# Performance work log

Hardware: AMD Instinct MI355X
Metric: run time of the kernel (lower is better)

The kernel has to match this reference:

```python
import jax, jax.numpy as jnp
import numpy as np

H_OUT, W_OUT = 473, 473  # original image size the logits are upsampled to
BN_EPS = 1e-5


def _conv(x, w, pad):
    return jax.lax.conv_general_dilated(
        x, w, window_strides=(1, 1), padding=[(pad, pad), (pad, pad)],
        dimension_numbers=('NCHW', 'OIHW', 'NCHW'))


def _bn(x, g, b):
    # BatchNorm2d in training mode: batch statistics over (N, H, W)
    m = jnp.mean(x, axis=(0, 2, 3), keepdims=True)
    v = jnp.var(x, axis=(0, 2, 3), keepdims=True)
    return (x - m) * jax.lax.rsqrt(v + BN_EPS) * g.reshape(1, -1, 1, 1) + b.reshape(1, -1, 1, 1)


def setup_inputs() -> dict:
    key = jax.random.key(0)
    ks = jax.random.split(key, 8)
    B, C, Hf, Wf, NC = 2, 256, 60, 60, 2
    return {
        'V_a': jax.random.normal(ks[0], (B, C, Hf, Wf), jnp.float32),
        'V_b': jax.random.normal(ks[1], (B, C, Hf, Wf), jnp.float32),
        'D_a': jax.random.normal(ks[2], (B, C, Hf, Wf), jnp.float32),
        'W_e': jax.random.normal(ks[3], (C, C), jnp.float32) * 0.02,
        'gate_w': jax.random.normal(ks[4], (1, C, 1, 1), jnp.float32) * 0.01,
        'conv1_w': jax.random.normal(ks[5], (C, 3 * C, 3, 3), jnp.float32) * 0.01,
        'conv2_w': jax.random.normal(ks[6], (C, 2 * C, 3, 3), jnp.float32) * 0.01,
        'bn1_g': jnp.ones((C,), jnp.float32),
        'bn1_b': jnp.zeros((C,), jnp.float32),
        'bn2_g': jnp.ones((C,), jnp.float32),
        'bn2_b': jnp.zeros((C,), jnp.float32),
        'cls1_w': jax.random.normal(ks[7], (NC, C, 1, 1), jnp.float32) * 0.01,
        'cls1_b': jnp.zeros((NC,), jnp.float32),
        'cls2_w': jax.random.normal(jax.random.fold_in(key, 9), (NC, C, 1, 1), jnp.float32) * 0.01,
        'cls2_b': jnp.zeros((NC,), jnp.float32),
    }


def reference(V_a, V_b, D_a, W_e, gate_w, conv1_w, conv2_w,
              bn1_g, bn1_b, bn2_g, bn2_b, cls1_w, cls1_b, cls2_w, cls2_b):
    B, C, Hf, Wf = V_a.shape
    N = Hf * Wf
    V_a_flat = V_a.reshape(B, C, N)
    V_b_flat = V_b.reshape(B, C, N)

    # linear_e on transposed A features, then affinity S = (A^T W^T) B
    weighted = jnp.einsum('bcn,dc->bnd', V_a_flat, W_e)        # [B, N, C]
    S = jnp.einsum('bnd,bdm->bnm', weighted, V_b_flat)         # [B, N, N]

    S_row = jax.nn.softmax(S, axis=1)                          # softmax over dim 1
    S_colT = jax.nn.softmax(jnp.swapaxes(S, 1, 2), axis=1)     # softmax of S^T over dim 1

    Z_b = jnp.einsum('bcn,bnm->bcm', V_a_flat, S_row)          # attended for view b
    Z_a = jnp.einsum('bcn,bnm->bcm', V_b_flat, S_colT)         # attended for view a

    att1 = Z_a.reshape(B, C, Hf, Wf)
    att2 = Z_b.reshape(B, C, Hf, Wf)

    # 1x1 sigmoid gates
    att1 = att1 * jax.nn.sigmoid(_conv(att1, gate_w, 0))
    att2 = att2 * jax.nn.sigmoid(_conv(att2, gate_w, 0))

    # conc1: branch-1 concatenates gated attention, RGB feat, and depth feat
    x1 = jnp.concatenate([att1, V_a, D_a], axis=1)             # [B, 3C, Hf, Wf]
    x2 = jnp.concatenate([att2, V_b], axis=1)                  # [B, 2C, Hf, Wf]

    x1 = jax.nn.relu(_bn(_conv(x1, conv1_w, 1), bn1_g, bn1_b))
    x2 = jax.nn.relu(_bn(_conv(x2, conv2_w, 1), bn2_g, bn2_b))

    x1 = _conv(x1, cls1_w, 0) + cls1_b.reshape(1, -1, 1, 1)
    x2 = _conv(x2, cls2_w, 0) + cls2_b.reshape(1, -1, 1, 1)

    NC = cls1_w.shape[0]
    x1 = jax.image.resize(x1, (B, NC, H_OUT, W_OUT), 'linear')
    x2 = jax.image.resize(x2, (B, NC, H_OUT, W_OUT), 'linear')
    return jax.nn.sigmoid(x1), jax.nn.sigmoid(x2)
```

## Files before the change

kernel.cpp:

```cpp
#include <hip/hip_runtime.h>

#define BB 2
#define CC 256
#define NN 3600
#define NCH 2
#define HO 473
#define WO 473
#define NR 3712
#define NTI 29
#define ZKI 29
#define ZKS 4
#define CZKS 3

typedef unsigned short u16;
typedef __attribute__((ext_vector_type(8))) short short8;
typedef __attribute__((ext_vector_type(4))) float f32x4;

static __device__ __forceinline__ u16 f2bf(float f) {
    unsigned u = __float_as_uint(f);
    unsigned r = (u + 0x7FFF + ((u >> 16) & 1)) >> 16;
    return (u16)r;
}
static __device__ __forceinline__ u16 f2h(float f) {
    _Float16 h = (_Float16)f;
    return __builtin_bit_cast(unsigned short, h);
}
static __device__ __forceinline__ float h2f(u16 u) {
    _Float16 h = __builtin_bit_cast(_Float16, u);
    return (float)h;
}

static __device__ __forceinline__ void glds16(const u16* g, u16* l) {
    __builtin_amdgcn_global_load_lds(
        (const __attribute__((address_space(1))) void*)g,
        (__attribute__((address_space(3))) void*)l, 16, 0, 0);
}


__global__ __launch_bounds__(256)
void gemm_we(const u16* __restrict__ vat, const u16* __restrict__ web,
             u16* __restrict__ wgtb)
{
    __shared__ u16 As[128 * 64];
    __shared__ u16 Bs[128 * 64];
    const u16* A = vat + (long)blockIdx.z * NR * CC;
    u16* Cp = wgtb + (long)blockIdx.z * NR * CC;

    const int t = threadIdx.x;
    const int w = t >> 6, lane = t & 63;
    const int mh = (w >> 1) * 64, nh = (w & 1) * 64;
    const int lm = lane & 15, quad = lane >> 4;
    const int m0 = blockIdx.y * 128, n0 = blockIdx.x * 128;
    const int wb = t & 192;

    f32x4 acc[4][4] = {};

    for (int k0 = 0; k0 < CC; k0 += 64) {
#pragma unroll
        for (int i = 0; i < 4; ++i) {
            int idx = i * 256 + t;
            int row = idx >> 3;
            int sc8 = ((idx ^ row) & 7) * 8;
            glds16(A + (long)(m0 + row) * CC + k0 + sc8, &As[(i * 256 + wb) * 8]);
            glds16(web + (long)(n0 + row) * CC + k0 + sc8, &Bs[(i * 256 + wb) * 8]);
        }
        __syncthreads();
#pragma unroll
        for (int s = 0; s < 2; ++s) {
            short8 a[4], b[4];
#pragma unroll
            for (int i = 0; i < 4; ++i)
                a[i] = *(const short8*)(&As[(mh + i * 16 + lm) * 64 + ((s * 4 + quad) ^ (lm & 7)) * 8]);
#pragma unroll
            for (int j = 0; j < 4; ++j)
                b[j] = *(const short8*)(&Bs[(nh + j * 16 + lm) * 64 + ((s * 4 + quad) ^ (lm & 7)) * 8]);
#pragma unroll
            for (int i = 0; i < 4; ++i)
#pragma unroll
                for (int j = 0; j < 4; ++j)
                    acc[i][j] = __builtin_amdgcn_mfma_f32_16x16x32_bf16(a[i], b[j], acc[i][j], 0, 0, 0);
        }
        __syncthreads();
    }
#pragma unroll
    for (int i = 0; i < 4; ++i)
#pragma unroll
        for (int r = 0; r < 4; ++r) {
            int row = m0 + mh + i * 16 + quad * 4 + r;
            if (row < NN)
#pragma unroll
                for (int j = 0; j < 4; ++j) {
                    int col = n0 + nh + j * 16 + lm;
                    if (col < CC) Cp[(long)row * CC + col] = f2bf(acc[i][j][r]);
                }
        }
}

__global__ __launch_bounds__(256)
void gemm_s_stats(const u16* __restrict__ A, const u16* __restrict__ B,
                  u16* __restrict__ Sh, u16* __restrict__ STh,
                  float* __restrict__ prowm, float* __restrict__ prows,
                  float* __restrict__ pcolm, float* __restrict__ pcols)
{
    __shared__ u16 smem[17408];
    u16* As = smem;
    u16* Bs = smem + 8192;

    const int t = threadIdx.x;
    const int w = t >> 6, lane = t & 63;
    const int mh = (w >> 1) * 64, nh = (w & 1) * 64;
    const int lm = lane & 15, quad = lane >> 4;
    const int m0 = blockIdx.y * 128, n0 = blockIdx.x * 128;
    const int wb = t & 192;

    f32x4 acc[4][4] = {};

    for (int k0 = 0; k0 < CC; k0 += 64) {
#pragma unroll
        for (int i = 0; i < 4; ++i) {
            int idx = i * 256 + t;
            int row = idx >> 3;
            int sc8 = ((idx ^ row) & 7) * 8;
            glds16(A + (long)(m0 + row) * CC + k0 + sc8, &As[(i * 256 + wb) * 8]);
            glds16(B + (long)(n0 + row) * CC + k0 + sc8, &Bs[(i * 256 + wb) * 8]);
        }
        __syncthreads();
#pragma unroll
        for (int s = 0; s < 2; ++s) {
            short8 a[4], b[4];
#pragma unroll
            for (int i = 0; i < 4; ++i)
                a[i] = *(const short8*)(&As[(mh + i * 16 + lm) * 64 + ((s * 4 + quad) ^ (lm & 7)) * 8]);
#pragma unroll
            for (int j = 0; j < 4; ++j)
                b[j] = *(const short8*)(&Bs[(nh + j * 16 + lm) * 64 + ((s * 4 + quad) ^ (lm & 7)) * 8]);
#pragma unroll
            for (int i = 0; i < 4; ++i)
#pragma unroll
                for (int j = 0; j < 4; ++j)
                    acc[i][j] = __builtin_amdgcn_mfma_f32_16x16x32_bf16(a[i], b[j], acc[i][j], 0, 0, 0);
        }
        __syncthreads();
    }

    u16* tr = smem;

#pragma unroll
    for (int i = 0; i < 4; ++i)
#pragma unroll
        for (int j = 0; j < 4; ++j)
#pragma unroll
            for (int r = 0; r < 4; ++r)
                tr[(mh + i * 16 + quad * 4 + r) * 136 + (nh + j * 16 + lm)] = f2h(acc[i][j][r]);
    __syncthreads();
    {
        int row = t >> 1, hf = t & 1;
        int ng = m0 + row;
        if (ng < NN) {
#pragma unroll
            for (int q = 0; q < 8; ++q) {
                int cb = n0 + hf * 64 + q * 8;
                if (cb < NN)
                    *(uint4*)(&Sh[(long)ng * NR + cb]) =
                        *(const uint4*)(&tr[row * 136 + hf * 64 + q * 8]);
            }
        }
    }
    __syncthreads();

    bool cval[4];
#pragma unroll
    for (int j = 0; j < 4; ++j) cval[j] = (n0 + nh + j * 16 + lm) < NN;

    float* sm = (float*)smem;
    float* rowm = sm;
    float* rows_ = sm + 256;
    float* colm = sm + 512;
    float* cols_ = sm + 768;

#pragma unroll
    for (int i = 0; i < 4; ++i)
#pragma unroll
        for (int r = 0; r < 4; ++r) {
            float m = -3.0e38f;
#pragma unroll
            for (int j = 0; j < 4; ++j) if (cval[j]) m = fmaxf(m, acc[i][j][r]);
            m = fmaxf(m, __shfl_xor(m, 1, 64));
            m = fmaxf(m, __shfl_xor(m, 2, 64));
            m = fmaxf(m, __shfl_xor(m, 4, 64));
            m = fmaxf(m, __shfl_xor(m, 8, 64));
            float s = 0.f;
#pragma unroll
            for (int j = 0; j < 4; ++j) if (cval[j]) s += __expf(acc[i][j][r] - m);
            s += __shfl_xor(s, 1, 64);
            s += __shfl_xor(s, 2, 64);
            s += __shfl_xor(s, 4, 64);
            s += __shfl_xor(s, 8, 64);
            if (lm == 0) {
                int rr = mh + i * 16 + quad * 4 + r;
                rowm[(w & 1) * 128 + rr] = m;
                rows_[(w & 1) * 128 + rr] = s;
            }
        }

#pragma unroll
    for (int j = 0; j < 4; ++j) {
        float m = -3.0e38f;
#pragma unroll
        for (int i = 0; i < 4; ++i)
#pragma unroll
            for (int r = 0; r < 4; ++r)
                if (m0 + mh + i * 16 + quad * 4 + r < NN) m = fmaxf(m, acc[i][j][r]);
        m = fmaxf(m, __shfl_xor(m, 16, 64));
        m = fmaxf(m, __shfl_xor(m, 32, 64));
        float s = 0.f;
#pragma unroll
        for (int i = 0; i < 4; ++i)
#pragma unroll
            for (int r = 0; r < 4; ++r)
                if (m0 + mh + i * 16 + quad * 4 + r < NN) s += __expf(acc[i][j][r] - m);
        s += __shfl_xor(s, 16, 64);
        s += __shfl_xor(s, 32, 64);
        if (quad == 0) {
            int ccl = nh + j * 16 + lm;
            colm[(w >> 1) * 128 + ccl] = m;
            cols_[(w >> 1) * 128 + ccl] = s;
        }
    }
    __syncthreads();

    if (t < 128) {
        float m1 = rowm[t], m2 = rowm[128 + t];
        float M = fmaxf(m1, m2);
        float s = rows_[t] * __expf(m1 - M) + rows_[128 + t] * __expf(m2 - M);
        if (m0 + t < NN) {
            prowm[(long)blockIdx.x * NR + m0 + t] = M;
            prows[(long)blockIdx.x * NR + m0 + t] = s;
        }
    } else {
        int c = t - 128;
        float m1 = colm[c], m2 = colm[128 + c];
        float M = fmaxf(m1, m2);
        float s = cols_[c] * __expf(m1 - M) + cols_[128 + c] * __expf(m2 - M);
        if (n0 + c < NN) {
            pcolm[(long)blockIdx.y * NR + n0 + c] = M;
            pcols[(long)blockIdx.y * NR + n0 + c] = s;
        }
    }

    __syncthreads();
#pragma unroll
    for (int i = 0; i < 4; ++i)
#pragma unroll
        for (int j = 0; j < 4; ++j)
#pragma unroll
            for (int r = 0; r < 4; ++r)
                tr[(nh + j * 16 + lm) * 136 + (mh + i * 16 + quad * 4 + r)] = f2h(acc[i][j][r]);
    __syncthreads();
    {
        int row = t >> 1, hf = t & 1;
        int mg = n0 + row;
        if (mg < NN) {
#pragma unroll
            for (int q = 0; q < 8; ++q) {
                int cb = m0 + hf * 64 + q * 8;
                if (cb < NN)
                    *(uint4*)(&STh[(long)mg * NR + cb]) =
                        *(const uint4*)(&tr[row * 136 + hf * 64 + q * 8]);
            }
        }
    }
}

__global__ __launch_bounds__(256)
void stats_final(const float* __restrict__ prm, const float* __restrict__ prs,
                 const float* __restrict__ pcm, const float* __restrict__ pcs,
                 float* __restrict__ rm, float* __restrict__ ri,
                 float* __restrict__ cm, float* __restrict__ ci)
{
    int i = blockIdx.x * 256 + threadIdx.x;
    if (i >= NN) return;
    const float* pm = blockIdx.y ? pcm : prm;
    const float* ps = blockIdx.y ? pcs : prs;
    float m = -3.0e38f, s = 0.f;
#pragma unroll 4
    for (int tI = 0; tI < NTI; ++tI) {
        float m2 = pm[(long)tI * NR + i], s2 = ps[(long)tI * NR + i];
        float M = fmaxf(m, m2);
        s = s * __expf(m - M) + s2 * __expf(m2 - M);
        m = M;
    }
    float inv = 1.f / s;
    if (blockIdx.y) { cm[i] = m; ci[i] = inv; }
    else            { rm[i] = m; ri[i] = inv; }
}

__global__ __launch_bounds__(256, 2)
void gemm_z_128(const u16* __restrict__ vab_b, const u16* __restrict__ vbb_b,
                const u16* __restrict__ STh, const u16* __restrict__ Sh,
                const float* __restrict__ rm, const float* __restrict__ ri,
                const float* __restrict__ cm, const float* __restrict__ ci,
                float* __restrict__ Zb_b, float* __restrict__ Za_b)
{
    __shared__ u16 As[128 * 128];
    __shared__ u16 Bs[128 * 128];

    const int t = threadIdx.x;
    const int w = t >> 6, lane = t & 63;
    const int mh = (w >> 1) * 64, nh = (w & 1) * 64;
    const int lm = lane & 15, quad = lane >> 4;
    const int n0 = blockIdx.x * 128;
    const int ks = blockIdx.y;
    const int zz = blockIdx.z;
    const int branch = zz & 1;
    const int m0 = (zz >> 1) * 128;
    const u16* A = branch ? vbb_b : vab_b;
    const u16* B = branch ? Sh : STh;
    const float* mxp = branch ? rm : cm;
    const float* isp = branch ? ri : ci;
    float* Cp = branch ? Za_b : Zb_b;
    const int wb = t & 192;

    const int base = ZKI / ZKS, rem = ZKI % ZKS;
    const int it0 = ks * base + (ks < rem ? ks : rem);
    const int itn = base + (ks < rem ? 1 : 0);

    int scv[8];
    const u16* Arow[8];
    const u16* Brow[8];
    float bm[8], bi[8];
#pragma unroll
    for (int i = 0; i < 8; ++i) {
        int idx = i * 256 + t;
        int row = idx >> 4, c = idx & 15;
        scv[i] = (c & 8) * 8 + ((c ^ row) & 7) * 8;
        Arow[i] = A + (long)(m0 + row) * NR + scv[i];
        int rg = n0 + row;
        Brow[i] = B + (long)rg * NR + scv[i];
        int rc = rg < NN ? rg : 0;
        bm[i] = mxp[rc];
        bi[i] = isp[rc];
    }

    f32x4 acc[4][4] = {};

    for (int it = it0; it < it0 + itn; ++it) {
        const int k0 = it * 128;
#pragma unroll
        for (int i = 0; i < 8; ++i)
            glds16(Arow[i] + k0, &As[(i * 256 + wb) * 8]);
#pragma unroll
        for (int i = 0; i < 8; ++i) {
            u16 o[8];
            uint4 v = *(const uint4*)(Brow[i] + k0);
            const u16* hp = (const u16*)&v;
            if (k0 + scv[i] < NN) {
#pragma unroll
                for (int e = 0; e < 8; ++e)
                    o[e] = f2bf(__expf(h2f(hp[e]) - bm[i]) * bi[i]);
            } else {
#pragma unroll
                for (int e = 0; e < 8; ++e) o[e] = 0;
            }
            *(uint4*)(&Bs[(i * 256 + t) * 8]) = *(const uint4*)o;
        }
        __syncthreads();
#pragma unroll
        for (int s = 0; s < 4; ++s) {
            const int sl = ((s >> 1) * 8 + (((s & 1) * 4 + quad) ^ (lm & 7))) * 8;
            short8 a[4], b[4];
#pragma unroll
            for (int i = 0; i < 4; ++i)
                a[i] = *(const short8*)(&As[(mh + i * 16 + lm) * 128 + sl]);
#pragma unroll
            for (int j = 0; j < 4; ++j)
                b[j] = *(const short8*)(&Bs[(nh + j * 16 + lm) * 128 + sl]);
#pragma unroll
            for (int i = 0; i < 4; ++i)
#pragma unroll
                for (int j = 0; j < 4; ++j)
                    acc[i][j] = __builtin_amdgcn_mfma_f32_16x16x32_bf16(a[i], b[j], acc[i][j], 0, 0, 0);
        }
        __syncthreads();
    }

#pragma unroll
    for (int i = 0; i < 4; ++i)
#pragma unroll
        for (int r = 0; r < 4; ++r) {
            int row = m0 + mh + i * 16 + quad * 4 + r;
#pragma unroll
            for (int j = 0; j < 4; ++j) {
                int col = n0 + nh + j * 16 + lm;
                if (col < NN)
                    atomicAdd(&Cp[(long)row * NN + col], acc[i][j][r]);
            }
        }
}

__global__ __launch_bounds__(256, 4)
void conv_both(const u16* __restrict__ W1, const u16* __restrict__ W2,
               const u16* __restrict__ gzaT, const u16* __restrict__ vat,
               const u16* __restrict__ daT, const u16* __restrict__ gzbT,
               const u16* __restrict__ vbt, const u16* __restrict__ zbuf,
               float* __restrict__ y1, float* __restrict__ y2)
{
    __shared__ u16 As[128 * 64];
    __shared__ u16 Bs[128 * 64];

    const int t = threadIdx.x;
    const int w = t >> 6, lane = t & 63;
    const int mh = (w >> 1) * 64, nh = (w & 1) * 64;
    const int lm = lane & 15, quad = lane >> 4;
    const int wb = t & 192;

    const long L = blockIdx.x + (long)NTI * (blockIdx.y + (long)CZKS * blockIdx.z);
    const int combo = (int)(L & 7);
    const long rest = L >> 3;
    const int ks = (int)(rest % CZKS);
    const int px = (int)(rest / CZKS);
    const int which = combo >> 2;
    const int b = (combo >> 1) & 1;
    const int m0 = (combo & 1) * 128;
    const int n0 = px * 128;

    const int CIN = which ? 512 : 768;
    const int KT = 9 * CIN;
    const u16* W = which ? W2 : W1;
    const u16* P0 = which ? gzbT : gzaT;
    const u16* P1 = which ? vbt : vat;
    const u16* P2 = which ? vbt : daT;
    float* Y = which ? y2 : y1;
    const long pstride = (long)NR * CC;

    const int PER = 3 * (CIN / 64);
    const int it0 = ks * PER;
    const int dh = ks - 1;

    int rowv[4], sc8v[4], rb[4];
    bool okd[4][3];
#pragma unroll
    for (int i = 0; i < 4; ++i) {
        int idx = i * 256 + t;
        int row = idx >> 3;
        rowv[i] = row;
        sc8v[i] = ((idx ^ row) & 7) * 8;
        int pq = n0 + row;
        int h = pq / 60, wp = pq - h * 60;
        rb[i] = (pq + dh * 60) * CC + sc8v[i];
        bool hok = (pq < NN) && ((unsigned)(h + dh) < 60u);
#pragma unroll
        for (int d = 0; d < 3; ++d)
            okd[i][d] = hok && ((unsigned)(wp + d - 1) < 60u);
    }

    f32x4 acc[4][4] = {};

    for (int it = it0; it < it0 + PER; ++it) {
        const int k0 = it * 64;
        const int g = it - it0;
        const int dw = g % 3;
        const int pc = g / 3;
        const int plane = pc >> 2;
        const int cip = (pc & 3) * 64;
        const u16* srcp = ((plane == 0) ? P0 : (plane == 1) ? P1 : P2)
                          + (long)b * pstride + cip;

#pragma unroll
        for (int i = 0; i < 4; ++i) {
            glds16(W + (long)(m0 + rowv[i]) * KT + k0 + sc8v[i], &As[(i * 256 + wb) * 8]);
            const u16* gs = okd[i][dw] ? srcp + rb[i] + (dw - 1) * CC : zbuf;
            glds16(gs, &Bs[(i * 256 + wb) * 8]);
        }
        __syncthreads();
#pragma unroll
        for (int s = 0; s < 2; ++s) {
            short8 a[4], bfr[4];
#pragma unroll
            for (int i = 0; i < 4; ++i)
                a[i] = *(const short8*)(&As[(mh + i * 16 + lm) * 64 + ((s * 4 + quad) ^ (lm & 7)) * 8]);
#pragma unroll
            for (int j = 0; j < 4; ++j)
                bfr[j] = *(const short8*)(&Bs[(nh + j * 16 + lm) * 64 + ((s * 4 + quad) ^ (lm & 7)) * 8]);
#pragma unroll
            for (int i = 0; i < 4; ++i)
#pragma unroll
                for (int j = 0; j < 4; ++j)
                    acc[i][j] = __builtin_amdgcn_mfma_f32_16x16x32_bf16(a[i], bfr[j], acc[i][j], 0, 0, 0);
        }
        __syncthreads();
    }

    float* out = Y + (long)b * CC * NN;
#pragma unroll
    for (int i = 0; i < 4; ++i)
#pragma unroll
        for (int r = 0; r < 4; ++r) {
            int row = m0 + mh + i * 16 + quad * 4 + r;
#pragma unroll
            for (int j = 0; j < 4; ++j) {
                int col = n0 + nh + j * 16 + lm;
                if (col < NN)
                    atomicAdd(&out[(long)row * NN + col], acc[i][j][r]);
            }
        }
}

__global__ __launch_bounds__(256)
void cvt_we(const float* __restrict__ W, u16* __restrict__ O)
{
    int i = blockIdx.x * 256 + threadIdx.x;
    if (i < CC * CC) O[i] = f2bf(W[i]);
}

__global__ __launch_bounds__(256)
void transpose_cvt3(const float* __restrict__ Va, const float* __restrict__ Vb,
                    const float* __restrict__ Da,
                    u16* __restrict__ vat, u16* __restrict__ vbt,
                    u16* __restrict__ daT,
                    u16* __restrict__ vab, u16* __restrict__ vbb)
{
    __shared__ float tile[64][65];
    int z = blockIdx.z;
    int s = z % 3, b = z / 3;
    const float* V = (s == 0) ? Va : (s == 1) ? Vb : Da;
    u16* VT = (s == 0) ? vat : (s == 1) ? vbt : daT;
    u16* Vpad = (s == 0) ? vab : (s == 1) ? vbb : nullptr;

    int c0 = blockIdx.y * 64, n0 = blockIdx.x * 64;
    int t = threadIdx.x;
#pragma unroll
    for (int e = 0; e < 16; ++e) {
        int f = e * 256 + t; int i = f >> 6, j = f & 63;
        int n = n0 + j;
        float v = 0.f;
        if (n < NN) v = V[((long)b * CC + c0 + i) * NN + n];
        tile[i][j] = v;
        if (Vpad) Vpad[((long)b * CC + c0 + i) * NR + n] = f2bf(v);
    }
    __syncthreads();
#pragma unroll
    for (int e = 0; e < 16; ++e) {
        int f = e * 256 + t; int i = f >> 6, j = f & 63;
        int n = n0 + i;
        if (n < NN) VT[((long)b * NR + n) * CC + c0 + j] = f2bf(tile[j][i]);
    }
}

__global__ __launch_bounds__(256)
void transpose_gate(const float* __restrict__ Za, const float* __restrict__ Zb,
                    const float* __restrict__ sga, const float* __restrict__ sgb,
                    u16* __restrict__ gzaT, u16* __restrict__ gzbT)
{
    __shared__ float tile[64][65];
    int z = blockIdx.z;
    int b = z & 1, ab = z >> 1;
    const float* Z = ab ? Zb : Za;
    const float* sg = ab ? sgb : sga;
    u16* ZT = ab ? gzbT : gzaT;

    int c0 = blockIdx.y * 64, n0 = blockIdx.x * 64;
    int t = threadIdx.x;
#pragma unroll
    for (int e = 0; e < 16; ++e) {
        int f = e * 256 + t; int i = f >> 6, j = f & 63;
        int n = n0 + j;
        float v = 0.f;
        if (n < NN) v = Z[((long)b * CC + c0 + i) * NN + n];
        tile[i][j] = v;
    }
    __syncthreads();
#pragma unroll
    for (int e = 0; e < 16; ++e) {
        int f = e * 256 + t; int i = f >> 6, j = f & 63;
        int n = n0 + i;
        if (n < NN)
            ZT[((long)b * NR + n) * CC + c0 + j] = f2bf(tile[j][i] * sg[b * NN + n]);
    }
}

template<int CIN>
__global__ __launch_bounds__(256)
void cvt_convw(const float* __restrict__ W, u16* __restrict__ O)
{
    const int KT = 9 * CIN;
    const int PER = 3 * (CIN / 64);
    long idx = (long)blockIdx.x * 256 + threadIdx.x;
    if (idx >= (long)CC * KT) return;
    int co = (int)(idx / KT);
    int r = (int)(idx % KT);
    int c64 = r >> 6, within = r & 63;
    int ks = c64 / PER, g = c64 % PER;
    int dw = g % 3, pc = g / 3;
    int tap = ks * 3 + dw;
    int ci = pc * 64 + within;
    O[idx] = f2bf(W[((long)co * CIN + ci) * 9 + tap]);
}

__global__ __launch_bounds__(256)
void gate_sig(const float* __restrict__ Za, const float* __restrict__ Zb,
              const float* __restrict__ gw,
              float* __restrict__ sga, float* __restrict__ sgb)
{
    int t = threadIdx.x;
    int px = t & 63, ck = t >> 6;
    int b = blockIdx.y;
    int ab = blockIdx.z;
    const float* Z = ab ? Zb : Za;
    float* sg = ab ? sgb : sga;
    int p = blockIdx.x * 64 + px;
    const float* Zp = Z + (long)b * CC * NN;
    float g = 0.f;
    if (p < NN) {
        for (int c = ck * 64; c < ck * 64 + 64; ++c) g += gw[c] * Zp[(long)c * NN + p];
    }
    __shared__ float red[256];
    red[t] = g;
    __syncthreads();
    if (t < 64) {
        int pp = blockIdx.x * 64 + t;
        if (pp < NN) {
            float tot = red[t] + red[t + 64] + red[t + 128] + red[t + 192];
            sg[b * NN + pp] = 1.f / (1.f + __expf(-tot));
        }
    }
}

__global__ __launch_bounds__(256)
void bn_stats_kernel(const float* __restrict__ y1, const float* __restrict__ y2,
                     const float* __restrict__ g1, const float* __restrict__ b1,
                     const float* __restrict__ g2, const float* __restrict__ b2,
                     float* __restrict__ sc1, float* __restrict__ sh1,
                     float* __restrict__ sc2, float* __restrict__ sh2)
{
    int which = blockIdx.x >> 8;
    int c = blockIdx.x & 255, t = threadIdx.x;
    const float* Y = which ? y2 : y1;
    const float* g = which ? g2 : g1;
    const float* beta = which ? b2 : b1;
    float* scale = which ? sc2 : sc1;
    float* shift = which ? sh2 : sh1;
    float s = 0.f, sq = 0.f;
    for (int b = 0; b < BB; ++b) {
        const float* p = Y + (long)b * CC * NN + (long)c * NN;
        for (int i = t; i < NN; i += 256) { float v = p[i]; s += v; sq += v * v; }
    }
    __shared__ float ls[256], lq[256];
    ls[t] = s; lq[t] = sq;
    __syncthreads();
    for (int off = 128; off > 0; off >>= 1) {
        if (t < off) { ls[t] += ls[t + off]; lq[t] += lq[t + off]; }
        __syncthreads();
    }
    if (t == 0) {
        const float inv = 1.f / (float)(BB * NN);
        float mean = ls[0] * inv;
        float var = fmaxf(lq[0] * inv - mean * mean, 0.f);
        float sc = g[c] * rsqrtf(var + 1e-5f);
        scale[c] = sc;
        shift[c] = beta[c] - mean * sc;
    }
}

__global__ __launch_bounds__(256)
void cls_kernel(const float* __restrict__ y1, const float* __restrict__ y2,
                const float* __restrict__ sc1, const float* __restrict__ sh1,
                const float* __restrict__ sc2, const float* __restrict__ sh2,
                const float* __restrict__ cw1, const float* __restrict__ cb1,
                const float* __restrict__ cw2, const float* __restrict__ cb2,
                float* __restrict__ O1, float* __restrict__ O2)
{
    int which = blockIdx.z;
    const float* Y = which ? y2 : y1;
    const float* scale = which ? sc2 : sc1;
    const float* shift = which ? sh2 : sh1;
    const float* cw = which ? cw2 : cw1;
    const float* cb = which ? cb2 : cb1;
    float* O = which ? O2 : O1;

    int t = threadIdx.x;
    int px = t & 63, ck = t >> 6;
    int b = blockIdx.y;
    int p = blockIdx.x * 64 + px;
    const float* Yb = Y + (long)b * CC * NN;
    float a0 = 0.f, a1 = 0.f;
    if (p < NN) {
        for (int c = ck * 64; c < ck * 64 + 64; ++c) {
            float v = Yb[(long)c * NN + p] * scale[c] + shift[c];
            v = fmaxf(v, 0.f);
            a0 += cw[c] * v;
            a1 += cw[CC + c] * v;
        }
    }
    __shared__ float r0[256], r1[256];
    r0[t] = a0; r1[t] = a1;
    __syncthreads();
    if (t < 64) {
        int pp = blockIdx.x * 64 + t;
        if (pp < NN) {
            float s0 = r0[t] + r0[t + 64] + r0[t + 128] + r0[t + 192];
            float s1 = r1[t] + r1[t + 64] + r1[t + 128] + r1[t + 192];
            O[(long)b * NCH * NN + pp] = s0 + cb[0];
            O[(long)b * NCH * NN + NN + pp] = s1 + cb[1];
        }
    }
}

__global__ __launch_bounds__(256)
void resize_sig_kernel(const float* __restrict__ I1, const float* __restrict__ I2,
                       float* __restrict__ O)
{
    const long HALF = (long)BB * NCH * HO * WO;
    long gid = (long)blockIdx.x * 256 + threadIdx.x;
    if (gid >= HALF) return;
    int half = blockIdx.y;
    const float* I = half ? I2 : I1;
    float* Op = O + half * HALF;

    int j = (int)(gid % WO);
    long r = gid / WO;
    int i = (int)(r % HO);
    int pc = (int)(r / HO);
    const float* ip = I + (long)pc * NN;

    const float SCL = 60.0f / 473.0f;
    float fy = (i + 0.5f) * SCL - 0.5f;
    float fx = (j + 0.5f) * SCL - 0.5f;
    int y0 = (int)floorf(fy);
    int x0 = (int)floorf(fx);
    float ty = fy - (float)y0;
    float tx = fx - (float)x0;
    int y0c = max(y0, 0), y1c = min(y0 + 1, 59);
    int x0c = max(x0, 0), x1c = min(x0 + 1, 59);
    float va = ip[y0c * 60 + x0c], vb = ip[y0c * 60 + x1c];
    float vc = ip[y1c * 60 + x0c], vd = ip[y1c * 60 + x1c];
    float v = (1.f - ty) * ((1.f - tx) * va + tx * vb) + ty * ((1.f - tx) * vc + tx * vd);
    Op[gid] = 1.f / (1.f + __expf(-v));
}

extern "C" void kernel_launch(void* const* d_in, const int* in_sizes, int n_in,
                              void* d_out, int out_size, void* d_ws, size_t ws_size,
                              hipStream_t stream)
{
    const float* V_a    = (const float*)d_in[0];
    const float* V_b    = (const float*)d_in[1];
    const float* D_a    = (const float*)d_in[2];
    const float* W_e    = (const float*)d_in[3];
    const float* gate_w = (const float*)d_in[4];
    const float* conv1_w = (const float*)d_in[5];
    const float* conv2_w = (const float*)d_in[6];
    const float* bn1_g = (const float*)d_in[7];
    const float* bn1_b = (const float*)d_in[8];
    const float* bn2_g = (const float*)d_in[9];
    const float* bn2_b = (const float*)d_in[10];
    const float* cls1_w = (const float*)d_in[11];
    const float* cls1_b = (const float*)d_in[12];
    const float* cls2_w = (const float*)d_in[13];
    const float* cls2_b = (const float*)d_in[14];
    float* out = (float*)d_out;

    size_t off = 0;
    char* wsb = (char*)d_ws;
    auto carve = [&](size_t bytes) -> char* {
        char* p = wsb + off; off += (bytes + 255) & ~(size_t)255; return p;
    };

    u16* Sh    = (u16*)carve((size_t)NR * NR * 2);
    u16* STh   = (u16*)carve((size_t)NR * NR * 2);
    u16* vab   = (u16*)carve((size_t)BB * CC * NR * 2);
    u16* vbb   = (u16*)carve((size_t)BB * CC * NR * 2);
    u16* vat   = (u16*)carve((size_t)BB * NR * CC * 2);
    u16* vbt   = (u16*)carve((size_t)BB * NR * CC * 2);
    u16* daT   = (u16*)carve((size_t)BB * NR * CC * 2);
    u16* gzaT  = (u16*)carve((size_t)BB * NR * CC * 2);
    u16* gzbT  = (u16*)carve((size_t)BB * NR * CC * 2);
    u16* wgtb  = (u16*)carve((size_t)BB * NR * CC * 2);
    u16* zbuf  = (u16*)carve(256);
    u16* web   = (u16*)carve((size_t)CC * CC * 2);
    u16* wt1   = (u16*)carve((size_t)CC * 9 * 768 * 2);
    u16* wt2   = (u16*)carve((size_t)CC * 9 * 512 * 2);
    float* Za  = (float*)carve((size_t)BB * CC * NN * 4);
    float* Zb  = (float*)carve((size_t)BB * CC * NN * 4);
    float* y1  = (float*)carve((size_t)BB * CC * NN * 4);
    float* y2  = (float*)carve((size_t)BB * CC * NN * 4);
    float* rmx = (float*)carve((size_t)BB * NN * 4);
    float* rsm = (float*)carve((size_t)BB * NN * 4);
    float* cmx = (float*)carve((size_t)BB * NN * 4);
    float* csm = (float*)carve((size_t)BB * NN * 4);
    float* sga = (float*)carve((size_t)BB * NN * 4);
    float* sgb = (float*)carve((size_t)BB * NN * 4);
    float* prm = (float*)carve((size_t)NTI * NR * 4);
    float* prs = (float*)carve((size_t)NTI * NR * 4);
    float* pcm = (float*)carve((size_t)NTI * NR * 4);
    float* pcs = (float*)carve((size_t)NTI * NR * 4);
    float* c1o = (float*)carve((size_t)BB * NCH * NN * 4);
    float* c2o = (float*)carve((size_t)BB * NCH * NN * 4);

    dim3 blk(256);

    hipMemsetAsync(Za, 0, (size_t)4 * BB * CC * NN * 4, stream);
    hipMemsetAsync(zbuf, 0, 256, stream);

    cvt_we<<<256, blk, 0, stream>>>(W_e, web);
    transpose_cvt3<<<dim3(58, 4, 3 * BB), blk, 0, stream>>>(
        V_a, V_b, D_a, vat, vbt, daT, vab, vbb);
    cvt_convw<768><<<(int)(((long)CC * 9 * 768 + 255) / 256), blk, 0, stream>>>(conv1_w, wt1);
    cvt_convw<512><<<(int)(((long)CC * 9 * 512 + 255) / 256), blk, 0, stream>>>(conv2_w, wt2);

    gemm_we<<<dim3(2, NTI, BB), blk, 0, stream>>>(vat, web, wgtb);

    for (int b = 0; b < BB; ++b) {
        const u16* wgtb_b = wgtb + (long)b * NR * CC;
        const u16* vbt_b  = vbt + (long)b * NR * CC;
        const u16* vab_b  = vab + (long)b * CC * NR;
        const u16* vbb_b  = vbb + (long)b * CC * NR;
        float* rmx_b = rmx + b * NN; float* rsm_b = rsm + b * NN;
        float* cmx_b = cmx + b * NN; float* csm_b = csm + b * NN;

        gemm_s_stats<<<dim3(NTI, NTI), blk, 0, stream>>>(
            wgtb_b, vbt_b, Sh, STh, prm, prs, pcm, pcs);
        stats_final<<<dim3((NN + 255) / 256, 2), blk, 0, stream>>>(
            prm, prs, pcm, pcs, rmx_b, rsm_b, cmx_b, csm_b);
        gemm_z_128<<<dim3(NTI, ZKS, 4), blk, 0, stream>>>(
            vab_b, vbb_b, STh, Sh, rmx_b, rsm_b, cmx_b, csm_b,
            Zb + (long)b * CC * NN, Za + (long)b * CC * NN);
    }

    gate_sig<<<dim3(57, BB, 2), blk, 0, stream>>>(Za, Zb, gate_w, sga, sgb);
    transpose_gate<<<dim3(57, 4, 2 * BB), blk, 0, stream>>>(Za, Zb, sga, sgb, gzaT, gzbT);

    conv_both<<<dim3(NTI, CZKS, 8), blk, 0, stream>>>(
        wt1, wt2, gzaT, vat, daT, gzbT, vbt, zbuf, y1, y2);

    bn_stats_kernel<<<2 * CC, blk, 0, stream>>>(
        y1, y2, bn1_g, bn1_b, bn2_g, bn2_b, rmx, rsm, cmx, csm);
    cls_kernel<<<dim3(57, BB, 2), blk, 0, stream>>>(
        y1, y2, rmx, rsm, cmx, csm, cls1_w, cls1_b, cls2_w, cls2_b, c1o, c2o);

    resize_sig_kernel<<<dim3((int)(((long)BB * NCH * HO * WO + 255) / 256), 2), blk, 0, stream>>>(c1o, c2o, out);
}
```

Before: 547.1 us.

## Double conv K-tile to 128 and fuse gate sigmoid with transpose kernel

The conv implicit-GEMM now loads 128-wide K slices (two 64-channel chunks per stage), which halves the number of barrier-separated iterations. The weight layout is reordered so the tap offset is the outer index, and launch bounds drop to 2 blocks per SM to fit the doubled LDS. Separately, the gate sigmoid and the transpose/scale kernels are merged into one kernel that computes the gate in shared memory, removing a launch and the sga/sgb round trip. The merged kernel has fewer blocks (57x4), each looping over all channels, so it has less parallelism and rereads Z for the gate.

```diff
diff --git a/kernel.cpp b/kernel.cpp
--- a/kernel.cpp
+++ b/kernel.cpp
@@ -398,15 +398,15 @@
         }
 }
 
-__global__ __launch_bounds__(256, 4)
+__global__ __launch_bounds__(256, 2)
 void conv_both(const u16* __restrict__ W1, const u16* __restrict__ W2,
                const u16* __restrict__ gzaT, const u16* __restrict__ vat,
                const u16* __restrict__ daT, const u16* __restrict__ gzbT,
                const u16* __restrict__ vbt, const u16* __restrict__ zbuf,
                float* __restrict__ y1, float* __restrict__ y2)
 {
-    __shared__ u16 As[128 * 64];
-    __shared__ u16 Bs[128 * 64];
+    __shared__ u16 As[128 * 128];
+    __shared__ u16 Bs[128 * 128];
 
     const int t = threadIdx.x;
     const int w = t >> 6, lane = t & 63;
@@ -426,6 +426,8 @@
 
     const int CIN = which ? 512 : 768;
     const int KT = 9 * CIN;
+    const int PCN2 = CIN >> 7;
+    const int PER2 = 3 * PCN2;
     const u16* W = which ? W2 : W1;
     const u16* P0 = which ? gzbT : gzaT;
     const u16* P1 = which ? vbt : vat;
@@ -433,55 +435,55 @@
     float* Y = which ? y2 : y1;
     const long pstride = (long)NR * CC;
 
-    const int PER = 3 * (CIN / 64);
-    const int it0 = ks * PER;
     const int dh = ks - 1;
-
-    int rowv[4], sc8v[4], rb[4];
-    bool okd[4][3];
-#pragma unroll
-    for (int i = 0; i < 4; ++i) {
-        int idx = i * 256 + t;
-        int row = idx >> 3;
-        rowv[i] = row;
-        sc8v[i] = ((idx ^ row) & 7) * 8;
-        int pq = n0 + row;
-        int h = pq / 60, wp = pq - h * 60;
-        rb[i] = (pq + dh * 60) * CC + sc8v[i];
-        bool hok = (pq < NN) && ((unsigned)(h + dh) < 60u);
+    const int half = (t >> 3) & 1;
+
+    long aoff[8];
+    int pb[8], okb[8];
+#pragma unroll
+    for (int i = 0; i < 8; ++i) {
+        int row = i * 16 + (t >> 4);
+        int slot8 = (((t & 7) ^ row) & 7) * 8;
+        aoff[i] = (long)(m0 + row) * KT + half * 64 + slot8;
+        int p = n0 + row;
+        int h = p / 60, wp = p - h * 60;
+        bool hok = (p < NN) && ((unsigned)(h + dh) < 60u);
+        int ob = 0;
 #pragma unroll
         for (int d = 0; d < 3; ++d)
-            okd[i][d] = hok && ((unsigned)(wp + d - 1) < 60u);
+            if (hok && ((unsigned)(wp + d - 1) < 60u)) ob |= (1 << d);
+        okb[i] = ob;
+        pb[i] = (p + dh * 60 - 1) * CC + slot8;
     }
 
     f32x4 acc[4][4] = {};
 
-    for (int it = it0; it < it0 + PER; ++it) {
-        const int k0 = it * 64;
-        const int g = it - it0;
-        const int dw = g % 3;
-        const int pc = g / 3;
-        const int plane = pc >> 2;
-        const int cip = (pc & 3) * 64;
-        const u16* srcp = ((plane == 0) ? P0 : (plane == 1) ? P1 : P2)
-                          + (long)b * pstride + cip;
-
-#pragma unroll
-        for (int i = 0; i < 4; ++i) {
-            glds16(W + (long)(m0 + rowv[i]) * KT + k0 + sc8v[i], &As[(i * 256 + wb) * 8]);
-            const u16* gs = okd[i][dw] ? srcp + rb[i] + (dw - 1) * CC : zbuf;
+    int dwi = 0, pcp = 0;
+    const long wslice = (long)ks * (3 * CIN);
+    for (int it = 0; it < PER2; ++it) {
+        const long k0 = wslice + (long)it * 128;
+        const int pcl = 2 * pcp + half;
+        const int plane = pcl >> 2;
+        const u16* sp = (plane == 0) ? P0 : (plane == 1) ? P1 : P2;
+        const u16* sbase = sp + (long)b * pstride + dwi * CC + ((pcl & 3) << 6);
+
+#pragma unroll
+        for (int i = 0; i < 8; ++i) {
+            glds16(W + aoff[i] + k0, &As[(i * 256 + wb) * 8]);
+            const u16* gs = ((okb[i] >> dwi) & 1) ? sbase + pb[i] : zbuf;
             glds16(gs, &Bs[(i * 256 + wb) * 8]);
         }
         __syncthreads();
 #pragma unroll
-        for (int s = 0; s < 2; ++s) {
+        for (int s = 0; s < 4; ++s) {
+            const int sl = ((s >> 1) * 8 + (((s & 1) * 4 + quad) ^ (lm & 7))) * 8;
             short8 a[4], bfr[4];
 #pragma unroll
             for (int i = 0; i < 4; ++i)
-                a[i] = *(const short8*)(&As[(mh + i * 16 + lm) * 64 + ((s * 4 + quad) ^ (lm & 7)) * 8]);
+                a[i] = *(const short8*)(&As[(mh + i * 16 + lm) * 128 + sl]);
 #pragma unroll
             for (int j = 0; j < 4; ++j)
-                bfr[j] = *(const short8*)(&Bs[(nh + j * 16 + lm) * 64 + ((s * 4 + quad) ^ (lm & 7)) * 8]);
+                bfr[j] = *(const short8*)(&Bs[(nh + j * 16 + lm) * 128 + sl]);
 #pragma unroll
             for (int i = 0; i < 4; ++i)
 #pragma unroll
@@ -489,6 +491,7 @@
                     acc[i][j] = __builtin_amdgcn_mfma_f32_16x16x32_bf16(a[i], bfr[j], acc[i][j], 0, 0, 0);
         }
         __syncthreads();
+        if (++pcp == PCN2) { pcp = 0; ++dwi; }
     }
 
     float* out = Y + (long)b * CC * NN;
@@ -547,81 +550,72 @@
     }
 }
 
-__global__ __launch_bounds__(256)
-void transpose_gate(const float* __restrict__ Za, const float* __restrict__ Zb,
-                    const float* __restrict__ sga, const float* __restrict__ sgb,
-                    u16* __restrict__ gzaT, u16* __restrict__ gzbT)
-{
-    __shared__ float tile[64][65];
-    int z = blockIdx.z;
-    int b = z & 1, ab = z >> 1;
-    const float* Z = ab ? Zb : Za;
-    const float* sg = ab ? sgb : sga;
-    u16* ZT = ab ? gzbT : gzaT;
-
-    int c0 = blockIdx.y * 64, n0 = blockIdx.x * 64;
-    int t = threadIdx.x;
-#pragma unroll
-    for (int e = 0; e < 16; ++e) {
-        int f = e * 256 + t; int i = f >> 6, j = f & 63;
-        int n = n0 + j;
-        float v = 0.f;
-        if (n < NN) v = Z[((long)b * CC + c0 + i) * NN + n];
-        tile[i][j] = v;
-    }
-    __syncthreads();
-#pragma unroll
-    for (int e = 0; e < 16; ++e) {
-        int f = e * 256 + t; int i = f >> 6, j = f & 63;
-        int n = n0 + i;
-        if (n < NN)
-            ZT[((long)b * NR + n) * CC + c0 + j] = f2bf(tile[j][i] * sg[b * NN + n]);
-    }
-}
-
 template<int CIN>
 __global__ __launch_bounds__(256)
 void cvt_convw(const float* __restrict__ W, u16* __restrict__ O)
 {
     const int KT = 9 * CIN;
-    const int PER = 3 * (CIN / 64);
+    const int PCN = CIN / 64;
+    const int PER = 3 * PCN;
     long idx = (long)blockIdx.x * 256 + threadIdx.x;
     if (idx >= (long)CC * KT) return;
     int co = (int)(idx / KT);
     int r = (int)(idx % KT);
     int c64 = r >> 6, within = r & 63;
     int ks = c64 / PER, g = c64 % PER;
-    int dw = g % 3, pc = g / 3;
+    int dw = g / PCN, pc = g % PCN;
     int tap = ks * 3 + dw;
     int ci = pc * 64 + within;
     O[idx] = f2bf(W[((long)co * CIN + ci) * 9 + tap]);
 }
 
 __global__ __launch_bounds__(256)
-void gate_sig(const float* __restrict__ Za, const float* __restrict__ Zb,
-              const float* __restrict__ gw,
-              float* __restrict__ sga, float* __restrict__ sgb)
-{
+void gate_transpose(const float* __restrict__ Za, const float* __restrict__ Zb,
+                    const float* __restrict__ gw,
+                    u16* __restrict__ gzaT, u16* __restrict__ gzbT)
+{
+    __shared__ float tile[64][65];
+    __shared__ float red[256];
+    __shared__ float sgs[64];
+
+    int zy = blockIdx.y;
+    int b = zy & 1, ab = zy >> 1;
+    const float* Z = ab ? Zb : Za;
+    u16* ZT = ab ? gzbT : gzaT;
+    int n0 = blockIdx.x * 64;
     int t = threadIdx.x;
     int px = t & 63, ck = t >> 6;
-    int b = blockIdx.y;
-    int ab = blockIdx.z;
-    const float* Z = ab ? Zb : Za;
-    float* sg = ab ? sgb : sga;
-    int p = blockIdx.x * 64 + px;
     const float* Zp = Z + (long)b * CC * NN;
+
     float g = 0.f;
+    int p = n0 + px;
     if (p < NN) {
         for (int c = ck * 64; c < ck * 64 + 64; ++c) g += gw[c] * Zp[(long)c * NN + p];
     }
-    __shared__ float red[256];
     red[t] = g;
     __syncthreads();
     if (t < 64) {
-        int pp = blockIdx.x * 64 + t;
-        if (pp < NN) {
-            float tot = red[t] + red[t + 64] + red[t + 128] + red[t + 192];
-            sg[b * NN + pp] = 1.f / (1.f + __expf(-tot));
+        float tot = red[t] + red[t + 64] + red[t + 128] + red[t + 192];
+        sgs[t] = 1.f / (1.f + __expf(-tot));
+    }
+
+    for (int c0 = 0; c0 < CC; c0 += 64) {
+        __syncthreads();
+#pragma unroll
+        for (int e = 0; e < 16; ++e) {
+            int f = e * 256 + t; int i = f >> 6, j = f & 63;
+            int n = n0 + j;
+            float v = 0.f;
+            if (n < NN) v = Zp[(long)(c0 + i) * NN + n];
+            tile[i][j] = v;
+        }
+        __syncthreads();
+#pragma unroll
+        for (int e = 0; e < 16; ++e) {
+            int f = e * 256 + t; int i = f >> 6, j = f & 63;
+            int n = n0 + i;
+            if (n < NN)
+                ZT[((long)b * NR + n) * CC + c0 + j] = f2bf(tile[j][i] * sgs[i]);
         }
     }
 }
@@ -787,8 +781,6 @@
     float* rsm = (float*)carve((size_t)BB * NN * 4);
     float* cmx = (float*)carve((size_t)BB * NN * 4);
     float* csm = (float*)carve((size_t)BB * NN * 4);
-    float* sga = (float*)carve((size_t)BB * NN * 4);
-    float* sgb = (float*)carve((size_t)BB * NN * 4);
     float* prm = (float*)carve((size_t)NTI * NR * 4);
     float* prs = (float*)carve((size_t)NTI * NR * 4);
     float* pcm = (float*)carve((size_t)NTI * NR * 4);
@@ -826,8 +818,8 @@
             Zb + (long)b * CC * NN, Za + (long)b * CC * NN);
     }
 
-    gate_sig<<<dim3(57, BB, 2), blk, 0, stream>>>(Za, Zb, gate_w, sga, sgb);
-    transpose_gate<<<dim3(57, 4, 2 * BB), blk, 0, stream>>>(Za, Zb, sga, sgb, gzaT, gzbT);
+    gate_transpose<<<dim3(57, 2 * BB), blk, 0, stream>>>(
+        Za, Zb, gate_w, gzaT, gzbT);
 
     conv_both<<<dim3(NTI, CZKS, 8), blk, 0, stream>>>(
         wt1, wt2, gzaT, vat, daT, gzbT, vbt, zbuf, y1, y2);
```

Measured after the change: 550.0 us. Within noise of the previous version (+0.5%).
